# Kernel optimization log

Hardware: AMD Instinct MI355X
Metric: run time of the kernel (lower is better)

Reference implementation:

```python
import jax, jax.numpy as jnp
import numpy as np

EXPERT_NUM = 8
TOPK = 2
N_EMBD = 768
D_FF = 3072
B, S = 2, 1024
T = B * S


def setup_inputs() -> dict:
    key = jax.random.key(0)
    ks = jax.random.split(key, 6)
    x = jax.random.normal(ks[0], (B, S, N_EMBD), dtype=jnp.float32)
    # gumbel noise, matching gumbel_noise(n, k) in the torch module
    u = jax.random.uniform(ks[1], (T, EXPERT_NUM), dtype=jnp.float32,
                           minval=1e-6, maxval=1.0 - 1e-6)
    noise = -jnp.log(-jnp.log(u))
    router_w = jax.random.normal(ks[2], (EXPERT_NUM, N_EMBD), dtype=jnp.float32) * (N_EMBD ** -0.5)
    w1 = jax.random.normal(ks[3], (EXPERT_NUM, N_EMBD, D_FF), dtype=jnp.float32) * (N_EMBD ** -0.5)
    b1 = jnp.zeros((EXPERT_NUM, D_FF), dtype=jnp.float32)
    w2 = jax.random.normal(ks[4], (EXPERT_NUM, D_FF, N_EMBD), dtype=jnp.float32) * (D_FF ** -0.5)
    b2 = jnp.zeros((EXPERT_NUM, N_EMBD), dtype=jnp.float32)
    return {"x": x, "noise": noise, "router_w": router_w,
            "w1": w1, "b1": b1, "w2": w2, "b2": b2}


def reference(x, noise, router_w, w1, b1, w2, b2):
    d = x.shape[-1]
    xs = x.reshape(-1, d)                                   # [T, d]
    gate_logits = xs @ router_w.T + noise                   # [T, E]
    # topk_exp > 1 branch: topk first, then softmax over the k kept logits
    weights, selected = jax.lax.top_k(gate_logits, TOPK)    # [T, k]
    weights = jax.nn.softmax(weights.astype(jnp.float32), axis=1).astype(x.dtype)
    out = jnp.zeros_like(xs)
    for e in range(EXPERT_NUM):
        # combine weight of expert e per token (0 where not selected)
        w_e = jnp.sum(jnp.where(selected == e, weights, 0.0), axis=1)  # [T]
        h = jax.nn.gelu(xs @ w1[e] + b1[e])                 # [T, d_ff]
        y = h @ w2[e] + b2[e]                               # [T, d]
        out = out + w_e[:, None] * y
    return out.reshape(x.shape)
```

## Files before the change

kernel.cpp:

```cpp
#include <hip/hip_runtime.h>
#include <hip/hip_bf16.h>

#define T_TOK 2048
#define NE 768
#define DFF 3072
#define NEXP 8
#define ROWS_PAD 4480
#define MAX_TILES 40

typedef __attribute__((ext_vector_type(8))) __bf16 bf16x8;
typedef __attribute__((ext_vector_type(4))) __bf16 bf16x4;
typedef __attribute__((ext_vector_type(4))) float f32x4;

__device__ __forceinline__ float gelu_tanh(float v) {
  float u = 0.7978845608028654f * (v + 0.044715f * v * v * v);
  float e = __expf(-2.0f * fabsf(u));
  float t = (1.0f - e) / (1.0f + e);
  t = copysignf(t, u);
  return 0.5f * v * (1.0f + t);
}

__global__ void router_kernel(const float* __restrict__ x,
                              const float* __restrict__ noise,
                              const float* __restrict__ rw,
                              int* __restrict__ sel, float* __restrict__ wgt) {
  int tok  = (blockIdx.x * blockDim.x + threadIdx.x) >> 6;
  int lane = threadIdx.x & 63;
  const float* xr = x + (size_t)tok * NE;
  float acc[NEXP];
#pragma unroll
  for (int e = 0; e < NEXP; e++) acc[e] = 0.f;
  for (int d = lane; d < NE; d += 64) {
    float xv = xr[d];
#pragma unroll
    for (int e = 0; e < NEXP; e++) acc[e] += xv * rw[e * NE + d];
  }
#pragma unroll
  for (int e = 0; e < NEXP; e++) {
#pragma unroll
    for (int off = 32; off > 0; off >>= 1) acc[e] += __shfl_xor(acc[e], off);
  }
  if (lane == 0) {
    float lg[NEXP];
#pragma unroll
    for (int e = 0; e < NEXP; e++) lg[e] = acc[e] + noise[tok * NEXP + e];
    int i0 = 0;
#pragma unroll
    for (int e = 1; e < NEXP; e++) if (lg[e] > lg[i0]) i0 = e;
    int i1 = (i0 == 0) ? 1 : 0;
#pragma unroll
    for (int e = 0; e < NEXP; e++) if (e != i0 && lg[e] > lg[i1]) i1 = e;
    float ex = __expf(lg[i1] - lg[i0]);
    float w0 = 1.f / (1.f + ex);
    sel[tok * 2]     = i0; sel[tok * 2 + 1] = i1;
    wgt[tok * 2]     = w0; wgt[tok * 2 + 1] = 1.f - w0;
  }
}

__global__ void assign_kernel(const int* __restrict__ sel,
                              int* __restrict__ offs, int* __restrict__ pair_tok,
                              int* __restrict__ slot_of, int* __restrict__ tiles,
                              int* __restrict__ ntl) {
  __shared__ int scnt[NEXP];
  __shared__ int soff[NEXP + 1];
  int e = threadIdx.x >> 6;
  int lane = threadIdx.x & 63;

  int count = 0;
  for (int t0 = 0; t0 < T_TOK; t0 += 64) {
    int t = t0 + lane;
    bool m = (sel[t * 2] == e) | (sel[t * 2 + 1] == e);
    count += __popcll(__ballot(m));
  }
  if (lane == 0) scnt[e] = count;
  __syncthreads();

  if (threadIdx.x == 0) {
    int s = 0;
    for (int k = 0; k < NEXP; k++) { soff[k] = s; s += scnt[k]; }
    soff[NEXP] = s;
    for (int i = 0; i <= NEXP; i++) offs[i] = soff[i];
    int k2 = 0;
    for (int k = 0; k < NEXP; k++)
      for (int r = soff[k]; r < soff[k + 1]; r += 128) {
        tiles[k2 * 2] = k; tiles[k2 * 2 + 1] = r; k2++;
      }
    *ntl = k2;
  }
  __syncthreads();

  int base = soff[e];
  for (int t0 = 0; t0 < T_TOK; t0 += 64) {
    int t = t0 + lane;
    int s0 = sel[t * 2], s1 = sel[t * 2 + 1];
    bool m0 = (s0 == e), m1 = (s1 == e);
    bool m = m0 | m1;
    unsigned long long mask = __ballot(m);
    int pos = __popcll(mask & ((1ull << lane) - 1ull));
    if (m) {
      int slot = base + pos;
      pair_tok[slot] = t;
      slot_of[t * 2 + (m0 ? 0 : 1)] = slot;
    }
    base += __popcll(mask);
  }
}

__global__ void gather_kernel(const float* __restrict__ x, const int* __restrict__ pair_tok,
                              __hip_bfloat16* __restrict__ xg) {
  int r = blockIdx.x;
  int tok = pair_tok[r];
  const float4* s = (const float4*)(x + (size_t)tok * NE);
  __hip_bfloat16* d = xg + (size_t)r * NE;
  int t = threadIdx.x;
  if (t < NE / 4) {
    float4 v = s[t];
    bf16x4 o;
    o[0] = (__bf16)__float2bfloat16(v.x); o[1] = (__bf16)__float2bfloat16(v.y);
    o[2] = (__bf16)__float2bfloat16(v.z); o[3] = (__bf16)__float2bfloat16(v.w);
    *reinterpret_cast<bf16x4*>(&d[t * 4]) = o;
  }
}

__global__ void transpose_cvt(const float* __restrict__ src, __hip_bfloat16* __restrict__ dst,
                              int K, int N) {
  __shared__ __hip_bfloat16 tile[64 * 72];
  int ntk = K >> 6, ntn = N >> 6;
  int bid = blockIdx.x;
  int e = bid / (ntk * ntn);
  int rem = bid % (ntk * ntn);
  int tk = rem / ntn, tn = rem % ntn;
  const float* s = src + (size_t)e * K * N + (size_t)(tk * 64) * N + tn * 64;
  int t = threadIdx.x;
  int a = t & 15;
  int kp = t >> 4;
#pragma unroll
  for (int i = 0; i < 2; i++) {
    int k = 2 * kp + 32 * i;
    float4 v0 = *reinterpret_cast<const float4*>(&s[(size_t)k * N + 4 * a]);
    float4 v1 = *reinterpret_cast<const float4*>(&s[(size_t)(k + 1) * N + 4 * a]);
    const float* p0 = &v0.x; const float* p1 = &v1.x;
#pragma unroll
    for (int j = 0; j < 4; j++) {
      __hip_bfloat162 p;
      p.x = __float2bfloat16(p0[j]); p.y = __float2bfloat16(p1[j]);
      *reinterpret_cast<__hip_bfloat162*>(&tile[(4 * a + j) * 72 + k]) = p;
    }
  }
  __syncthreads();
  int n = t >> 3, g = t & 7;
  __hip_bfloat16* d = dst + (size_t)e * N * K + (size_t)(tn * 64) * K + tk * 64;
#pragma unroll
  for (int i = 0; i < 2; i++) {
    int row = n + 32 * i;
    bf16x8 v = *reinterpret_cast<const bf16x8*>(&tile[row * 72 + g * 8]);
    *reinterpret_cast<bf16x8*>(&d[(size_t)row * K + g * 8]) = v;
  }
}

__device__ __forceinline__ int swz_chunk(int c) {
  return (c & ~7) | ((c & 7) ^ ((c >> 3) & 7));
}

template <int K, int N, int MODE, int SPLITS>
__global__ __launch_bounds__(256) void ffn_gemm(
    const __hip_bfloat16* __restrict__ A, const __hip_bfloat16* __restrict__ Bt,
    const float* __restrict__ bias, __hip_bfloat16* __restrict__ DST,
    const int* __restrict__ offs, const int* __restrict__ tiles,
    const int* __restrict__ ntl) {
  constexpr int NT = N / 128;
  constexpr int KS = K / SPLITS;
  constexpr int NS = KS / 32;
  int bid = blockIdx.x;
  int nt = bid % NT;
  int r1 = bid / NT;
  int sp = r1 % SPLITS;
  int ti = r1 / SPLITS;
  if (ti >= *ntl) return;
  int e = tiles[ti * 2], row0 = tiles[ti * 2 + 1];
  int rend = offs[e + 1];
  int n0 = nt * 128;
  int kbeg = sp * KS;

  __shared__ __align__(16) __hip_bfloat16 lds[3][2][128 * 32];

  int tid = threadIdx.x;
  int w = tid >> 6, l = tid & 63;
  int wr = w >> 1, wc = w & 1;
  int r16 = l & 15, q = l >> 4;

  f32x4 acc[4][4];
#pragma unroll
  for (int m = 0; m < 4; m++)
#pragma unroll
    for (int n = 0; n < 4; n++) acc[m][n] = (f32x4){0.f, 0.f, 0.f, 0.f};

  const __hip_bfloat16* Bte = Bt + (size_t)e * N * K;

  auto STAGE = [&](int b, int k0) {
    char* cA = (char*)lds[b][0];
    char* cB = (char*)lds[b][1];
#pragma unroll
    for (int i = 0; i < 2; i++) {
      int Lc = tid + 256 * i;
      int fc = swz_chunk(Lc);
      int row = fc >> 2, p = fc & 3;
      const __hip_bfloat16* ga = A + (size_t)(row0 + row) * K + k0 + p * 8;
      __builtin_amdgcn_global_load_lds(
          (const __attribute__((address_space(1))) void*)ga,
          (__attribute__((address_space(3))) void*)(cA + Lc * 16), 16, 0, 0);
    }
#pragma unroll
    for (int i = 0; i < 2; i++) {
      int Lc = tid + 256 * i;
      int fc = swz_chunk(Lc);
      int row = fc >> 2, p = fc & 3;
      const __hip_bfloat16* gb = Bte + (size_t)(n0 + row) * K + k0 + p * 8;
      __builtin_amdgcn_global_load_lds(
          (const __attribute__((address_space(1))) void*)gb,
          (__attribute__((address_space(3))) void*)(cB + Lc * 16), 16, 0, 0);
    }
  };

  STAGE(0, kbeg);
  if (NS > 1) STAGE(1, kbeg + 32);
  for (int t = 0; t < NS; t++) {
    if (t + 2 < NS) {
      STAGE((t + 2) % 3, kbeg + (t + 2) * 32);
      asm volatile("s_waitcnt vmcnt(8)" ::: "memory");
    } else if (t + 1 < NS) {
      asm volatile("s_waitcnt vmcnt(4)" ::: "memory");
    } else {
      asm volatile("s_waitcnt vmcnt(0)" ::: "memory");
    }
    __builtin_amdgcn_s_barrier();
    __builtin_amdgcn_sched_barrier(0);
    const char* cA = (const char*)lds[t % 3][0];
    const char* cB = (const char*)lds[t % 3][1];
    bf16x8 aF[4], bF[4];
#pragma unroll
    for (int m = 0; m < 4; m++) {
      int row = wr * 64 + m * 16 + r16;
      aF[m] = *reinterpret_cast<const bf16x8*>(cA + swz_chunk(row * 4 + q) * 16);
    }
#pragma unroll
    for (int n = 0; n < 4; n++) {
      int row = wc * 64 + n * 16 + r16;
      bF[n] = *reinterpret_cast<const bf16x8*>(cB + swz_chunk(row * 4 + q) * 16);
    }
#pragma unroll
    for (int m = 0; m < 4; m++)
#pragma unroll
      for (int n = 0; n < 4; n++)
        acc[m][n] = __builtin_amdgcn_mfma_f32_16x16x32_bf16(aF[m], bF[n], acc[m][n], 0, 0, 0);
    __builtin_amdgcn_s_barrier();
  }

  float* ldsF = (float*)&lds[0][0][0];
  __hip_bfloat16* dst = DST + (size_t)sp * ROWS_PAD * N;
#pragma unroll
  for (int hh = 0; hh < 2; hh++) {
    __syncthreads();
    if (wr == hh) {
#pragma unroll
      for (int m = 0; m < 4; m++)
#pragma unroll
        for (int n = 0; n < 4; n++)
#pragma unroll
          for (int rg = 0; rg < 4; rg++)
            ldsF[(m * 16 + q * 4 + rg) * 132 + wc * 64 + n * 16 + r16] = acc[m][n][rg];
    }
    __syncthreads();
#pragma unroll
    for (int i = 0; i < 4; i++) {
      int s = tid + 256 * i;
      int r = s >> 4, c8 = s & 15;
      int rr = row0 + hh * 64 + r;
      if (rr < rend) {
        const float* src = &ldsF[r * 132 + c8 * 8];
        float4 v0 = *reinterpret_cast<const float4*>(src);
        float4 v1 = *reinterpret_cast<const float4*>(src + 4);
        const float* bp = &bias[e * N + n0 + c8 * 8];
        float4 bb0 = *reinterpret_cast<const float4*>(bp);
        float4 bb1 = *reinterpret_cast<const float4*>(bp + 4);
        float vv[8]  = {v0.x, v0.y, v0.z, v0.w, v1.x, v1.y, v1.z, v1.w};
        float bbv[8] = {bb0.x, bb0.y, bb0.z, bb0.w, bb1.x, bb1.y, bb1.z, bb1.w};
        bf16x8 o;
#pragma unroll
        for (int j = 0; j < 8; j++) {
          float val;
          if (MODE == 0) val = gelu_tanh(vv[j] + bbv[j]);
          else           val = vv[j] + (sp == 0 ? bbv[j] : 0.f);
          o[j] = (__bf16)__float2bfloat16(val);
        }
        *reinterpret_cast<bf16x8*>(&dst[(size_t)rr * N + n0 + c8 * 8]) = o;
      }
    }
  }
}

template <int SPLITS>
__global__ void combine_kernel(const __hip_bfloat16* __restrict__ yb,
                               const int* __restrict__ slot_of,
                               const float* __restrict__ wgt,
                               float* __restrict__ out) {
  int t = blockIdx.x;
  int d = threadIdx.x;
  int s0 = slot_of[2 * t], s1 = slot_of[2 * t + 1];
  float w0 = wgt[2 * t], w1 = wgt[2 * t + 1];
  float a0 = 0.f, a1 = 0.f, a2 = 0.f, a3 = 0.f;
#pragma unroll
  for (int sp = 0; sp < SPLITS; sp++) {
    bf16x4 p = reinterpret_cast<const bf16x4*>(yb + (size_t)(sp * ROWS_PAD + s0) * NE)[d];
    bf16x4 r = reinterpret_cast<const bf16x4*>(yb + (size_t)(sp * ROWS_PAD + s1) * NE)[d];
    a0 += w0 * (float)p[0] + w1 * (float)r[0];
    a1 += w0 * (float)p[1] + w1 * (float)r[1];
    a2 += w0 * (float)p[2] + w1 * (float)r[2];
    a3 += w0 * (float)p[3] + w1 * (float)r[3];
  }
  float4 o = {a0, a1, a2, a3};
  reinterpret_cast<float4*>(out)[(size_t)t * (NE / 4) + d] = o;
}

extern "C" void kernel_launch(void* const* d_in, const int* in_sizes, int n_in,
                              void* d_out, int out_size, void* d_ws, size_t ws_size,
                              hipStream_t stream) {
  const float* x     = (const float*)d_in[0];
  const float* noise = (const float*)d_in[1];
  const float* rw    = (const float*)d_in[2];
  const float* w1    = (const float*)d_in[3];
  const float* b1    = (const float*)d_in[4];
  const float* w2    = (const float*)d_in[5];
  const float* b2    = (const float*)d_in[6];
  float* out = (float*)d_out;

  constexpr int SP2 = 2;

  char* ws = (char*)d_ws;
  size_t off = 0;
  auto carve = [&](size_t bytes) { void* p = ws + off; off = (off + bytes + 255) & ~255ull; return p; };
  int*   offs     = (int*)carve((NEXP + 1) * 4);
  int*   sel      = (int*)carve(T_TOK * 2 * 4);
  float* wgt      = (float*)carve(T_TOK * 2 * 4);
  int*   pair_tok = (int*)carve(ROWS_PAD * 4);
  int*   slot_of  = (int*)carve(T_TOK * 2 * 4);
  int*   tiles    = (int*)carve(MAX_TILES * 2 * 4);
  int*   ntl      = (int*)carve(4);
  __hip_bfloat16* xg  = (__hip_bfloat16*)carve((size_t)ROWS_PAD * NE * 2);
  __hip_bfloat16* h   = (__hip_bfloat16*)carve((size_t)ROWS_PAD * DFF * 2);
  __hip_bfloat16* yb  = (__hip_bfloat16*)carve((size_t)SP2 * ROWS_PAD * NE * 2);
  __hip_bfloat16* wt  = (__hip_bfloat16*)carve((size_t)NEXP * NE * DFF * 2);

  if (off > ws_size) {
    hipMemsetAsync(d_out, 0, (size_t)out_size * sizeof(float), stream);
    return;
  }

  router_kernel<<<(T_TOK * 64) / 256, 256, 0, stream>>>(x, noise, rw, sel, wgt);
  assign_kernel<<<1, 512, 0, stream>>>(sel, offs, pair_tok, slot_of, tiles, ntl);
  gather_kernel<<<T_TOK * 2, 256, 0, stream>>>(x, pair_tok, xg);

  transpose_cvt<<<NEXP * (NE / 64) * (DFF / 64), 256, 0, stream>>>(w1, wt, NE, DFF);
  ffn_gemm<NE, DFF, 0, 1><<<MAX_TILES * 1 * (DFF / 128), 256, 0, stream>>>(
      xg, wt, b1, h, offs, tiles, ntl);

  transpose_cvt<<<NEXP * (DFF / 64) * (NE / 64), 256, 0, stream>>>(w2, wt, DFF, NE);
  ffn_gemm<DFF, NE, 1, SP2><<<MAX_TILES * SP2 * (NE / 128), 256, 0, stream>>>(
      h, wt, b2, yb, offs, tiles, ntl);

  combine_kernel<SP2><<<T_TOK, 192, 0, stream>>>(yb, slot_of, wgt, out);
}
```

Baseline: 154.7 us.

## Fuse weight transposes into router and GEMM1 launches, widen GEMM N tile

Co-schedules the w1 transpose with the router kernel and the w2 transpose with the first expert GEMM, using block-index dispatch inside merged kernels so independent work overlaps and fewer launches are needed. GEMM tiles grow from 128x128 to 128x256, with 32 accumulators per wave and a larger LDS footprint. The second GEMM's split-K goes from 2 to 4, and its partial outputs reuse the wt1 buffer. Risks: the 72KB shared allocation and heavier register use lower occupancy, and the fused transpose blocks also reserve that much LDS.

```diff
diff --git a/kernel.cpp b/kernel.cpp
--- a/kernel.cpp
+++ b/kernel.cpp
@@ -7,6 +7,10 @@
 #define NEXP 8
 #define ROWS_PAD 4480
 #define MAX_TILES 40
+#define NB_G1 (MAX_TILES * 12)
+#define NB_T2 (NEXP * (DFF / 64) * (NE / 64))
+#define NB_RT 512
+#define NB_T1 (NEXP * (NE / 64) * (DFF / 64))
 
 typedef __attribute__((ext_vector_type(8))) __bf16 bf16x8;
 typedef __attribute__((ext_vector_type(4))) __bf16 bf16x4;
@@ -20,11 +24,16 @@
   return 0.5f * v * (1.0f + t);
 }
 
-__global__ void router_kernel(const float* __restrict__ x,
-                              const float* __restrict__ noise,
-                              const float* __restrict__ rw,
-                              int* __restrict__ sel, float* __restrict__ wgt) {
-  int tok  = (blockIdx.x * blockDim.x + threadIdx.x) >> 6;
+__device__ __forceinline__ int swz_chunk(int c) {
+  return (c & ~7) | ((c & 7) ^ ((c >> 3) & 7));
+}
+
+__device__ __forceinline__ void router_body(const float* __restrict__ x,
+                                            const float* __restrict__ noise,
+                                            const float* __restrict__ rw,
+                                            int* __restrict__ sel, float* __restrict__ wgt,
+                                            int bid) {
+  int tok  = (bid * 256 + (int)threadIdx.x) >> 6;
   int lane = threadIdx.x & 63;
   const float* xr = x + (size_t)tok * NE;
   float acc[NEXP];
@@ -55,6 +64,185 @@
     sel[tok * 2]     = i0; sel[tok * 2 + 1] = i1;
     wgt[tok * 2]     = w0; wgt[tok * 2 + 1] = 1.f - w0;
   }
+}
+
+__device__ __forceinline__ void transpose_body(const float* __restrict__ src,
+                                               __hip_bfloat16* __restrict__ dst,
+                                               int K, int N, int bid, char* smem) {
+  __hip_bfloat16* tile = (__hip_bfloat16*)smem;
+  int ntk = K >> 6, ntn = N >> 6;
+  int e = bid / (ntk * ntn);
+  int rem = bid % (ntk * ntn);
+  int tk = rem / ntn, tn = rem % ntn;
+  const float* s = src + (size_t)e * K * N + (size_t)(tk * 64) * N + tn * 64;
+  int t = threadIdx.x;
+  int a = t & 15;
+  int kp = t >> 4;
+#pragma unroll
+  for (int i = 0; i < 2; i++) {
+    int k = 2 * kp + 32 * i;
+    float4 v0 = *reinterpret_cast<const float4*>(&s[(size_t)k * N + 4 * a]);
+    float4 v1 = *reinterpret_cast<const float4*>(&s[(size_t)(k + 1) * N + 4 * a]);
+    const float* p0 = &v0.x; const float* p1 = &v1.x;
+#pragma unroll
+    for (int j = 0; j < 4; j++) {
+      __hip_bfloat162 p;
+      p.x = __float2bfloat16(p0[j]); p.y = __float2bfloat16(p1[j]);
+      *reinterpret_cast<__hip_bfloat162*>(&tile[(4 * a + j) * 72 + k]) = p;
+    }
+  }
+  __syncthreads();
+  int n = t >> 3, g = t & 7;
+  __hip_bfloat16* d = dst + (size_t)e * N * K + (size_t)(tn * 64) * K + tk * 64;
+#pragma unroll
+  for (int i = 0; i < 2; i++) {
+    int row = n + 32 * i;
+    bf16x8 v = *reinterpret_cast<const bf16x8*>(&tile[row * 72 + g * 8]);
+    *reinterpret_cast<bf16x8*>(&d[(size_t)row * K + g * 8]) = v;
+  }
+}
+
+template <int K, int N, int MODE, int SPLITS>
+__device__ __forceinline__ void gemm_body(
+    const __hip_bfloat16* __restrict__ A, const __hip_bfloat16* __restrict__ Bt,
+    const float* __restrict__ bias, __hip_bfloat16* __restrict__ DST,
+    const int* __restrict__ offs, const int* __restrict__ tiles,
+    const int* __restrict__ ntl, char* smem, int bid) {
+  constexpr int NT = N / 256;
+  constexpr int KS = K / SPLITS;
+  constexpr int NS = KS / 32;
+  int nt = bid % NT;
+  int r1 = bid / NT;
+  int sp = r1 % SPLITS;
+  int ti = r1 / SPLITS;
+  if (ti >= *ntl) return;
+  int e = tiles[ti * 2], row0 = tiles[ti * 2 + 1];
+  int rend = offs[e + 1];
+  int n0 = nt * 256;
+  int kbeg = sp * KS;
+
+  int tid = threadIdx.x;
+  int w = tid >> 6, l = tid & 63;
+  int wr = w >> 1, wc = w & 1;
+  int r16 = l & 15, q = l >> 4;
+
+  f32x4 acc[4][8];
+#pragma unroll
+  for (int m = 0; m < 4; m++)
+#pragma unroll
+    for (int n = 0; n < 8; n++) acc[m][n] = (f32x4){0.f, 0.f, 0.f, 0.f};
+
+  const __hip_bfloat16* Bte = Bt + (size_t)e * N * K;
+
+  auto STAGE = [&](int b, int k0) {
+    char* cA = smem + b * 24576;
+    char* cB = cA + 8192;
+#pragma unroll
+    for (int i = 0; i < 2; i++) {
+      int Lc = tid + 256 * i;
+      int fc = swz_chunk(Lc);
+      int row = fc >> 2, p = fc & 3;
+      const __hip_bfloat16* ga = A + (size_t)(row0 + row) * K + k0 + p * 8;
+      __builtin_amdgcn_global_load_lds(
+          (const __attribute__((address_space(1))) void*)ga,
+          (__attribute__((address_space(3))) void*)(cA + Lc * 16), 16, 0, 0);
+    }
+#pragma unroll
+    for (int i = 0; i < 4; i++) {
+      int Lc = tid + 256 * i;
+      int fc = swz_chunk(Lc);
+      int row = fc >> 2, p = fc & 3;
+      const __hip_bfloat16* gb = Bte + (size_t)(n0 + row) * K + k0 + p * 8;
+      __builtin_amdgcn_global_load_lds(
+          (const __attribute__((address_space(1))) void*)gb,
+          (__attribute__((address_space(3))) void*)(cB + Lc * 16), 16, 0, 0);
+    }
+  };
+
+  STAGE(0, kbeg);
+  if (NS > 1) STAGE(1, kbeg + 32);
+  for (int t = 0; t < NS; t++) {
+    if (t + 2 < NS) {
+      STAGE((t + 2) % 3, kbeg + (t + 2) * 32);
+      asm volatile("s_waitcnt vmcnt(12)" ::: "memory");
+    } else if (t + 1 < NS) {
+      asm volatile("s_waitcnt vmcnt(6)" ::: "memory");
+    } else {
+      asm volatile("s_waitcnt vmcnt(0)" ::: "memory");
+    }
+    __builtin_amdgcn_s_barrier();
+    __builtin_amdgcn_sched_barrier(0);
+    const char* cA = smem + (t % 3) * 24576;
+    const char* cB = cA + 8192;
+    bf16x8 aF[4], bF[8];
+#pragma unroll
+    for (int m = 0; m < 4; m++) {
+      int row = wr * 64 + m * 16 + r16;
+      aF[m] = *reinterpret_cast<const bf16x8*>(cA + swz_chunk(row * 4 + q) * 16);
+    }
+#pragma unroll
+    for (int n = 0; n < 8; n++) {
+      int row = wc * 128 + n * 16 + r16;
+      bF[n] = *reinterpret_cast<const bf16x8*>(cB + swz_chunk(row * 4 + q) * 16);
+    }
+#pragma unroll
+    for (int m = 0; m < 4; m++)
+#pragma unroll
+      for (int n = 0; n < 8; n++)
+        acc[m][n] = __builtin_amdgcn_mfma_f32_16x16x32_bf16(aF[m], bF[n], acc[m][n], 0, 0, 0);
+    __builtin_amdgcn_s_barrier();
+  }
+
+  float* ldsF = (float*)smem;
+  __hip_bfloat16* dst = DST + (size_t)sp * ROWS_PAD * N;
+#pragma unroll
+  for (int hh = 0; hh < 2; hh++) {
+    __syncthreads();
+    if (wr == hh) {
+#pragma unroll
+      for (int m = 0; m < 4; m++)
+#pragma unroll
+        for (int n = 0; n < 8; n++)
+#pragma unroll
+          for (int rg = 0; rg < 4; rg++)
+            ldsF[(m * 16 + q * 4 + rg) * 264 + wc * 128 + n * 16 + r16] = acc[m][n][rg];
+    }
+    __syncthreads();
+#pragma unroll
+    for (int i = 0; i < 8; i++) {
+      int s = tid + 256 * i;
+      int r = s >> 5, c8 = s & 31;
+      int rr = row0 + hh * 64 + r;
+      if (rr < rend) {
+        const float* src = &ldsF[r * 264 + c8 * 8];
+        float4 v0 = *reinterpret_cast<const float4*>(src);
+        float4 v1 = *reinterpret_cast<const float4*>(src + 4);
+        const float* bp = &bias[e * N + n0 + c8 * 8];
+        float4 bb0 = *reinterpret_cast<const float4*>(bp);
+        float4 bb1 = *reinterpret_cast<const float4*>(bp + 4);
+        float vv[8]  = {v0.x, v0.y, v0.z, v0.w, v1.x, v1.y, v1.z, v1.w};
+        float bbv[8] = {bb0.x, bb0.y, bb0.z, bb0.w, bb1.x, bb1.y, bb1.z, bb1.w};
+        bf16x8 o;
+#pragma unroll
+        for (int j = 0; j < 8; j++) {
+          float val;
+          if (MODE == 0) val = gelu_tanh(vv[j] + bbv[j]);
+          else           val = vv[j] + (sp == 0 ? bbv[j] : 0.f);
+          o[j] = (__bf16)__float2bfloat16(val);
+        }
+        *reinterpret_cast<bf16x8*>(&dst[(size_t)rr * N + n0 + c8 * 8]) = o;
+      }
+    }
+  }
+}
+
+__global__ __launch_bounds__(256) void router_t1_kernel(
+    const float* __restrict__ x, const float* __restrict__ noise,
+    const float* __restrict__ rw, int* __restrict__ sel, float* __restrict__ wgt,
+    const float* __restrict__ w1, __hip_bfloat16* __restrict__ wt1) {
+  __shared__ __align__(16) char smem[9216];
+  if (blockIdx.x < NB_RT) router_body(x, noise, rw, sel, wgt, blockIdx.x);
+  else transpose_body(w1, wt1, NE, DFF, blockIdx.x - NB_RT, smem);
 }
 
 __global__ void assign_kernel(const int* __restrict__ sel,
@@ -122,181 +310,26 @@
   }
 }
 
-__global__ void transpose_cvt(const float* __restrict__ src, __hip_bfloat16* __restrict__ dst,
-                              int K, int N) {
-  __shared__ __hip_bfloat16 tile[64 * 72];
-  int ntk = K >> 6, ntn = N >> 6;
-  int bid = blockIdx.x;
-  int e = bid / (ntk * ntn);
-  int rem = bid % (ntk * ntn);
-  int tk = rem / ntn, tn = rem % ntn;
-  const float* s = src + (size_t)e * K * N + (size_t)(tk * 64) * N + tn * 64;
-  int t = threadIdx.x;
-  int a = t & 15;
-  int kp = t >> 4;
-#pragma unroll
-  for (int i = 0; i < 2; i++) {
-    int k = 2 * kp + 32 * i;
-    float4 v0 = *reinterpret_cast<const float4*>(&s[(size_t)k * N + 4 * a]);
-    float4 v1 = *reinterpret_cast<const float4*>(&s[(size_t)(k + 1) * N + 4 * a]);
-    const float* p0 = &v0.x; const float* p1 = &v1.x;
-#pragma unroll
-    for (int j = 0; j < 4; j++) {
-      __hip_bfloat162 p;
-      p.x = __float2bfloat16(p0[j]); p.y = __float2bfloat16(p1[j]);
-      *reinterpret_cast<__hip_bfloat162*>(&tile[(4 * a + j) * 72 + k]) = p;
-    }
-  }
-  __syncthreads();
-  int n = t >> 3, g = t & 7;
-  __hip_bfloat16* d = dst + (size_t)e * N * K + (size_t)(tn * 64) * K + tk * 64;
-#pragma unroll
-  for (int i = 0; i < 2; i++) {
-    int row = n + 32 * i;
-    bf16x8 v = *reinterpret_cast<const bf16x8*>(&tile[row * 72 + g * 8]);
-    *reinterpret_cast<bf16x8*>(&d[(size_t)row * K + g * 8]) = v;
-  }
-}
-
-__device__ __forceinline__ int swz_chunk(int c) {
-  return (c & ~7) | ((c & 7) ^ ((c >> 3) & 7));
-}
-
-template <int K, int N, int MODE, int SPLITS>
-__global__ __launch_bounds__(256) void ffn_gemm(
-    const __hip_bfloat16* __restrict__ A, const __hip_bfloat16* __restrict__ Bt,
-    const float* __restrict__ bias, __hip_bfloat16* __restrict__ DST,
+__global__ __launch_bounds__(256) void g1_t2_kernel(
+    const __hip_bfloat16* __restrict__ xg, const __hip_bfloat16* __restrict__ wt1,
+    const float* __restrict__ b1, __hip_bfloat16* __restrict__ h,
+    const int* __restrict__ offs, const int* __restrict__ tiles,
+    const int* __restrict__ ntl,
+    const float* __restrict__ w2, __hip_bfloat16* __restrict__ wt2) {
+  __shared__ __align__(16) char smem[73728];
+  if (blockIdx.x < NB_G1)
+    gemm_body<NE, DFF, 0, 1>(xg, wt1, b1, h, offs, tiles, ntl, smem, blockIdx.x);
+  else
+    transpose_body(w2, wt2, DFF, NE, blockIdx.x - NB_G1, smem);
+}
+
+__global__ __launch_bounds__(256) void g2_kernel(
+    const __hip_bfloat16* __restrict__ h, const __hip_bfloat16* __restrict__ wt2,
+    const float* __restrict__ b2, __hip_bfloat16* __restrict__ yb,
     const int* __restrict__ offs, const int* __restrict__ tiles,
     const int* __restrict__ ntl) {
-  constexpr int NT = N / 128;
-  constexpr int KS = K / SPLITS;
-  constexpr int NS = KS / 32;
-  int bid = blockIdx.x;
-  int nt = bid % NT;
-  int r1 = bid / NT;
-  int sp = r1 % SPLITS;
-  int ti = r1 / SPLITS;
-  if (ti >= *ntl) return;
-  int e = tiles[ti * 2], row0 = tiles[ti * 2 + 1];
-  int rend = offs[e + 1];
-  int n0 = nt * 128;
-  int kbeg = sp * KS;
-
-  __shared__ __align__(16) __hip_bfloat16 lds[3][2][128 * 32];
-
-  int tid = threadIdx.x;
-  int w = tid >> 6, l = tid & 63;
-  int wr = w >> 1, wc = w & 1;
-  int r16 = l & 15, q = l >> 4;
-
-  f32x4 acc[4][4];
-#pragma unroll
-  for (int m = 0; m < 4; m++)
-#pragma unroll
-    for (int n = 0; n < 4; n++) acc[m][n] = (f32x4){0.f, 0.f, 0.f, 0.f};
-
-  const __hip_bfloat16* Bte = Bt + (size_t)e * N * K;
-
-  auto STAGE = [&](int b, int k0) {
-    char* cA = (char*)lds[b][0];
-    char* cB = (char*)lds[b][1];
-#pragma unroll
-    for (int i = 0; i < 2; i++) {
-      int Lc = tid + 256 * i;
-      int fc = swz_chunk(Lc);
-      int row = fc >> 2, p = fc & 3;
-      const __hip_bfloat16* ga = A + (size_t)(row0 + row) * K + k0 + p * 8;
-      __builtin_amdgcn_global_load_lds(
-          (const __attribute__((address_space(1))) void*)ga,
-          (__attribute__((address_space(3))) void*)(cA + Lc * 16), 16, 0, 0);
-    }
-#pragma unroll
-    for (int i = 0; i < 2; i++) {
-      int Lc = tid + 256 * i;
-      int fc = swz_chunk(Lc);
-      int row = fc >> 2, p = fc & 3;
-      const __hip_bfloat16* gb = Bte + (size_t)(n0 + row) * K + k0 + p * 8;
-      __builtin_amdgcn_global_load_lds(
-          (const __attribute__((address_space(1))) void*)gb,
-          (__attribute__((address_space(3))) void*)(cB + Lc * 16), 16, 0, 0);
-    }
-  };
-
-  STAGE(0, kbeg);
-  if (NS > 1) STAGE(1, kbeg + 32);
-  for (int t = 0; t < NS; t++) {
-    if (t + 2 < NS) {
-      STAGE((t + 2) % 3, kbeg + (t + 2) * 32);
-      asm volatile("s_waitcnt vmcnt(8)" ::: "memory");
-    } else if (t + 1 < NS) {
-      asm volatile("s_waitcnt vmcnt(4)" ::: "memory");
-    } else {
-      asm volatile("s_waitcnt vmcnt(0)" ::: "memory");
-    }
-    __builtin_amdgcn_s_barrier();
-    __builtin_amdgcn_sched_barrier(0);
-    const char* cA = (const char*)lds[t % 3][0];
-    const char* cB = (const char*)lds[t % 3][1];
-    bf16x8 aF[4], bF[4];
-#pragma unroll
-    for (int m = 0; m < 4; m++) {
-      int row = wr * 64 + m * 16 + r16;
-      aF[m] = *reinterpret_cast<const bf16x8*>(cA + swz_chunk(row * 4 + q) * 16);
-    }
-#pragma unroll
-    for (int n = 0; n < 4; n++) {
-      int row = wc * 64 + n * 16 + r16;
-      bF[n] = *reinterpret_cast<const bf16x8*>(cB + swz_chunk(row * 4 + q) * 16);
-    }
-#pragma unroll
-    for (int m = 0; m < 4; m++)
-#pragma unroll
-      for (int n = 0; n < 4; n++)
-        acc[m][n] = __builtin_amdgcn_mfma_f32_16x16x32_bf16(aF[m], bF[n], acc[m][n], 0, 0, 0);
-    __builtin_amdgcn_s_barrier();
-  }
-
-  float* ldsF = (float*)&lds[0][0][0];
-  __hip_bfloat16* dst = DST + (size_t)sp * ROWS_PAD * N;
-#pragma unroll
-  for (int hh = 0; hh < 2; hh++) {
-    __syncthreads();
-    if (wr == hh) {
-#pragma unroll
-      for (int m = 0; m < 4; m++)
-#pragma unroll
-        for (int n = 0; n < 4; n++)
-#pragma unroll
-          for (int rg = 0; rg < 4; rg++)
-            ldsF[(m * 16 + q * 4 + rg) * 132 + wc * 64 + n * 16 + r16] = acc[m][n][rg];
-    }
-    __syncthreads();
-#pragma unroll
-    for (int i = 0; i < 4; i++) {
-      int s = tid + 256 * i;
-      int r = s >> 4, c8 = s & 15;
-      int rr = row0 + hh * 64 + r;
-      if (rr < rend) {
-        const float* src = &ldsF[r * 132 + c8 * 8];
-        float4 v0 = *reinterpret_cast<const float4*>(src);
-        float4 v1 = *reinterpret_cast<const float4*>(src + 4);
-        const float* bp = &bias[e * N + n0 + c8 * 8];
-        float4 bb0 = *reinterpret_cast<const float4*>(bp);
-        float4 bb1 = *reinterpret_cast<const float4*>(bp + 4);
-        float vv[8]  = {v0.x, v0.y, v0.z, v0.w, v1.x, v1.y, v1.z, v1.w};
-        float bbv[8] = {bb0.x, bb0.y, bb0.z, bb0.w, bb1.x, bb1.y, bb1.z, bb1.w};
-        bf16x8 o;
-#pragma unroll
-        for (int j = 0; j < 8; j++) {
-          float val;
-          if (MODE == 0) val = gelu_tanh(vv[j] + bbv[j]);
-          else           val = vv[j] + (sp == 0 ? bbv[j] : 0.f);
-          o[j] = (__bf16)__float2bfloat16(val);
-        }
-        *reinterpret_cast<bf16x8*>(&dst[(size_t)rr * N + n0 + c8 * 8]) = o;
-      }
-    }
-  }
+  __shared__ __align__(16) char smem[73728];
+  gemm_body<DFF, NE, 1, 4>(h, wt2, b2, yb, offs, tiles, ntl, smem, blockIdx.x);
 }
 
 template <int SPLITS>
@@ -334,7 +367,7 @@
   const float* b2    = (const float*)d_in[6];
   float* out = (float*)d_out;
 
-  constexpr int SP2 = 2;
+  constexpr int SP2 = 4;
 
   char* ws = (char*)d_ws;
   size_t off = 0;
@@ -348,25 +381,22 @@
   int*   ntl      = (int*)carve(4);
   __hip_bfloat16* xg  = (__hip_bfloat16*)carve((size_t)ROWS_PAD * NE * 2);
   __hip_bfloat16* h   = (__hip_bfloat16*)carve((size_t)ROWS_PAD * DFF * 2);
-  __hip_bfloat16* yb  = (__hip_bfloat16*)carve((size_t)SP2 * ROWS_PAD * NE * 2);
-  __hip_bfloat16* wt  = (__hip_bfloat16*)carve((size_t)NEXP * NE * DFF * 2);
+  __hip_bfloat16* wt1 = (__hip_bfloat16*)carve((size_t)NEXP * NE * DFF * 2);
+  __hip_bfloat16* wt2 = (__hip_bfloat16*)carve((size_t)NEXP * NE * DFF * 2);
+  __hip_bfloat16* yb  = wt1;
 
   if (off > ws_size) {
     hipMemsetAsync(d_out, 0, (size_t)out_size * sizeof(float), stream);
     return;
   }
 
-  router_kernel<<<(T_TOK * 64) / 256, 256, 0, stream>>>(x, noise, rw, sel, wgt);
+  router_t1_kernel<<<NB_RT + NB_T1, 256, 0, stream>>>(x, noise, rw, sel, wgt, w1, wt1);
   assign_kernel<<<1, 512, 0, stream>>>(sel, offs, pair_tok, slot_of, tiles, ntl);
   gather_kernel<<<T_TOK * 2, 256, 0, stream>>>(x, pair_tok, xg);
 
-  transpose_cvt<<<NEXP * (NE / 64) * (DFF / 64), 256, 0, stream>>>(w1, wt, NE, DFF);
-  ffn_gemm<NE, DFF, 0, 1><<<MAX_TILES * 1 * (DFF / 128), 256, 0, stream>>>(
-      xg, wt, b1, h, offs, tiles, ntl);
-
-  transpose_cvt<<<NEXP * (DFF / 64) * (NE / 64), 256, 0, stream>>>(w2, wt, DFF, NE);
-  ffn_gemm<DFF, NE, 1, SP2><<<MAX_TILES * SP2 * (NE / 128), 256, 0, stream>>>(
-      h, wt, b2, yb, offs, tiles, ntl);
+  g1_t2_kernel<<<NB_G1 + NB_T2, 256, 0, stream>>>(xg, wt1, b1, h, offs, tiles, ntl, w2, wt2);
+
+  g2_kernel<<<MAX_TILES * SP2 * 3, 256, 0, stream>>>(h, wt2, b2, yb, offs, tiles, ntl);
 
   combine_kernel<SP2><<<T_TOK, 192, 0, stream>>>(yb, slot_of, wgt, out);
 }
```

Result: slower. 162.0 us (+4.8%).
